# Kernel tuning notes

Measured on AMD Instinct MI355X. Metric: run time of the kernel, lower is better.

The kernel has to match this reference:

```python
import jax, jax.numpy as jnp
import numpy as np

NUM_HEADS = 32
NUM_KV_HEADS = 8
HEAD_DIM = 128
WINDOW = 512
NUM_META = 4


def _swa_sink_mask(S):
    # allowed = causal & (within sliding window OR sink/meta token)
    i = jnp.arange(S)[:, None]   # q_idx
    j = jnp.arange(S)[None, :]   # kv_idx
    return (i >= j) & (((i - j) <= WINDOW) | (j < NUM_META))


def setup_inputs() -> dict:
    key = jax.random.key(0)
    k1, k2, k3 = jax.random.split(key, 3)
    B, S = 1, 2048
    return {
        "query_states": jax.random.normal(k1, (B, S, NUM_HEADS * HEAD_DIM), dtype=jnp.float32),
        "key_states": jax.random.normal(k2, (B, S, NUM_KV_HEADS * HEAD_DIM), dtype=jnp.float32),
        "value_states": jax.random.normal(k3, (B, S, NUM_KV_HEADS * HEAD_DIM), dtype=jnp.float32),
    }


def reference(query_states, key_states, value_states):
    B, S, _ = query_states.shape
    n_rep = NUM_HEADS // NUM_KV_HEADS
    # [B, H, S, D]
    q = query_states.reshape(B, S, NUM_HEADS, HEAD_DIM).transpose(0, 2, 1, 3)
    k = key_states.reshape(B, S, NUM_KV_HEADS, HEAD_DIM).transpose(0, 2, 1, 3)
    v = value_states.reshape(B, S, NUM_KV_HEADS, HEAD_DIM).transpose(0, 2, 1, 3)
    # repeat_kv: interleaved repeat along head dim (GQA)
    k = jnp.repeat(k, n_rep, axis=1)
    v = jnp.repeat(v, n_rep, axis=1)

    scale = 1.0 / jnp.sqrt(jnp.float32(HEAD_DIM))  # flex_attention default scale
    scores = jnp.einsum("bhqd,bhkd->bhqk", q, k) * scale
    mask = _swa_sink_mask(S)  # [S, S], every row has q_idx==kv_idx allowed
    scores = jnp.where(mask[None, None], scores, -jnp.inf)
    attn = jax.nn.softmax(scores, axis=-1)
    out = jnp.einsum("bhqk,bhkd->bhqd", attn, v)
    return out.transpose(0, 2, 1, 3).reshape(B, S, NUM_HEADS * HEAD_DIM)
```

## Files before the change

kernel.cpp:

```cpp
#include <hip/hip_runtime.h>
#include <math.h>

typedef __attribute__((ext_vector_type(8))) short bf16x8;
typedef __attribute__((ext_vector_type(16))) float f32x16;

#define WIN 512
#define META 4
#define QSCALE (0.08838834764831845f * 1.4426950408889634f)
#define MFIX2 20.197730572445487f

union U8 { int4 i4; bf16x8 bf; };

static __device__ __forceinline__ unsigned bf16_rne(float x) {
  unsigned u = __float_as_uint(x);
  return (u + 0x7FFFu + ((u >> 16) & 1u)) >> 16;
}
static __device__ __forceinline__ unsigned pk2_rne(float a, float b) {
  return bf16_rne(a) | (bf16_rne(b) << 16);
}
static __device__ __forceinline__ unsigned pk2_tr(float a, float b) {
  return (__float_as_uint(a) >> 16) | (__float_as_uint(b) & 0xFFFF0000u);
}
static __device__ __forceinline__ void gload16(const void* g, void* l) {
  __builtin_amdgcn_global_load_lds(
      (const __attribute__((address_space(1))) unsigned int*)g,
      (__attribute__((address_space(3))) unsigned int*)l, 16, 0, 0);
}

__global__ __launch_bounds__(256) void swa_prep(
    const float* __restrict__ Kg, const float* __restrict__ Vg,
    unsigned short* __restrict__ Kw, unsigned short* __restrict__ Vw)
{
  __shared__ float Kf[64][132];
  __shared__ float Vf[64][132];
  const int tid = threadIdx.x;
  const int hk = blockIdx.x & 7, tj = blockIdx.x >> 3;
  const int j0 = tj * 64;
  const int krow = tid >> 5;
  const int f4c = tid & 31;
  #pragma unroll
  for (int r = 0; r < 8; ++r) {
    const int key = r * 8 + krow;
    *(float4*)&Kf[key][f4c * 4] =
        *(const float4*)(Kg + (size_t)(j0 + key) * 1024 + hk * 128 + f4c * 4);
    *(float4*)&Vf[key][f4c * 4] =
        *(const float4*)(Vg + (size_t)(j0 + key) * 1024 + hk * 128 + f4c * 4);
  }
  __syncthreads();
  unsigned short* kout = Kw + ((size_t)(hk * 32 + tj)) * 8192;
  #pragma unroll
  for (int p = 0; p < 4; ++p) {
    const int gid = p * 256 + tid;
    const int s = gid >> 6, key = gid & 63;
    const float* src = &Kf[key][s * 8];
    *(int4*)(kout + gid * 8) = make_int4(
        (int)pk2_tr(src[0], src[1]), (int)pk2_tr(src[2], src[3]),
        (int)pk2_tr(src[4], src[5]), (int)pk2_tr(src[6], src[7]));
  }
  unsigned short* vout = Vw + ((size_t)(hk * 32 + tj)) * 8192;
  #pragma unroll
  for (int p = 0; p < 4; ++p) {
    const int fid = p * 256 + tid;
    const int c = fid >> 7, dim = fid & 127;
    const int kb = 16 * (c >> 1) + 4 * (c & 1);
    *(int4*)(vout + fid * 8) = make_int4(
        (int)pk2_tr(Vf[kb + 0][dim], Vf[kb + 1][dim]),
        (int)pk2_tr(Vf[kb + 2][dim], Vf[kb + 3][dim]),
        (int)pk2_tr(Vf[kb + 8][dim], Vf[kb + 9][dim]),
        (int)pk2_tr(Vf[kb + 10][dim], Vf[kb + 11][dim]));
  }
}

__global__ __launch_bounds__(512, 2) void swa_fused(
    const float* __restrict__ Qg, const unsigned short* __restrict__ Kw,
    const unsigned short* __restrict__ Vw, float* __restrict__ Og)
{
  __shared__ __align__(16) unsigned short KsB[2][8192];
  __shared__ __align__(16) unsigned short VtB[3][8192];

  const int tid = threadIdx.x;
  const int lane = tid & 63, wid = tid >> 6;
  const int cl = lane & 31, hl = lane >> 5;
  const int bid = blockIdx.x;
  const int hk = bid & 7;
  const int bq = bid >> 3;
  const int q0 = bq << 6;
  const int h = hk * 4 + (wid & 3);
  const int qw0 = q0 + ((wid >> 2) << 5);

  int4 qf[8];
  {
    const float* qrow = Qg + (size_t)(qw0 + cl) * 4096 + h * 128 + hl * 8;
    #pragma unroll
    for (int kc = 0; kc < 8; ++kc) {
      float4 x = *(const float4*)(qrow + kc * 16);
      float4 y = *(const float4*)(qrow + kc * 16 + 4);
      qf[kc] = make_int4(pk2_rne(x.x*QSCALE, x.y*QSCALE), pk2_rne(x.z*QSCALE, x.w*QSCALE),
                         pk2_rne(y.x*QSCALE, y.y*QSCALE), pk2_rne(y.z*QSCALE, y.w*QSCALE));
    }
  }

  f32x16 acc[4];
  #pragma unroll
  for (int nt = 0; nt < 4; ++nt)
    #pragma unroll
    for (int i = 0; i < 16; ++i) acc[nt][i] = 0.f;
  float lpA = 0.f, lpB = 0.f;

  const int jstart = (q0 > WIN) ? ((q0 - WIN) & ~63) : 0;
  const int sink = (jstart > 0) ? 1 : 0;
  const int niter = ((q0 + 63 - jstart) >> 6) + 1 + sink;
  const int tj0 = jstart >> 6;

  auto stage = [&](const int tj, unsigned short* kd, unsigned short* vd) {
    const size_t base = ((size_t)(hk * 32 + tj)) << 14;
    const char* ks = (const char*)Kw + base + tid * 16;
    gload16(ks, (char*)kd + tid * 16);
    gload16(ks + 8192, (char*)kd + tid * 16 + 8192);
    const char* vs = (const char*)Vw + base + tid * 16;
    gload16(vs, (char*)vd + tid * 16);
    gload16(vs + 8192, (char*)vd + tid * 16 + 8192);
  };

  #define MKA(P, o) make_int4( \
      (int)__builtin_amdgcn_perm(P[(o)+1], P[(o)+0], 0x07060302u), \
      (int)__builtin_amdgcn_perm(P[(o)+3], P[(o)+2], 0x07060302u), \
      (int)__builtin_amdgcn_perm(P[(o)+5], P[(o)+4], 0x07060302u), \
      (int)__builtin_amdgcn_perm(P[(o)+7], P[(o)+6], 0x07060302u))

  auto pv4 = [&](const unsigned short* Vb, const int kc, const int4 aw) {
    U8 a; a.i4 = aw;
    #pragma unroll
    for (int nt = 0; nt < 4; ++nt) {
      U8 b; b.i4 = *(const int4*)(Vb + kc * 2048 + hl * 1024 + nt * 256 + cl * 8);
      acc[nt] = __builtin_amdgcn_mfma_f32_32x32x16_bf16(a.bf, b.bf, acc[nt], 0, 0, 0);
    }
  };

  unsigned pu1[16];
  #pragma unroll
  for (int i = 0; i < 16; ++i) pu1[i] = 0u;

  stage(sink ? 0 : tj0, KsB[0], VtB[0]);
  __syncthreads();

  const unsigned short *kCur = KsB[0], *kNxt = KsB[1];
  const unsigned short *vPrv = VtB[2], *vCur = VtB[0], *vNxt = VtB[1];

  for (int t = 0; t < niter; ++t) {
    const bool isSink = (sink != 0) && (t == 0);
    const int jt = isSink ? 0 : jstart + ((t - sink) << 6);
    const bool needMask = (jt + 63 > qw0) || (qw0 + 31 - jt > WIN);

    if (t + 1 < niter)
      stage(tj0 + (t + 1 - sink), (unsigned short*)kNxt, (unsigned short*)vNxt);

    if (t > sink) {
      __builtin_amdgcn_s_setprio(1);
      pv4(vPrv, 2, MKA(pu1, 0));
      pv4(vPrv, 3, MKA(pu1, 8));
      __builtin_amdgcn_s_setprio(0);
    }

    f32x16 s0v, s1v;
    #pragma unroll
    for (int i = 0; i < 16; ++i) { s0v[i] = 0.f; s1v[i] = 0.f; }
    __builtin_amdgcn_s_setprio(1);
    if (isSink) {
      #pragma unroll
      for (int kc = 0; kc < 8; ++kc) {
        U8 b; b.i4 = qf[kc];
        U8 a0; a0.i4 = *(const int4*)(kCur + kc * 1024 + hl * 512 + cl * 8);
        s0v = __builtin_amdgcn_mfma_f32_32x32x16_bf16(a0.bf, b.bf, s0v, 0, 0, 0);
      }
    } else {
      #pragma unroll
      for (int kc = 0; kc < 8; ++kc) {
        U8 b; b.i4 = qf[kc];
        U8 a0; a0.i4 = *(const int4*)(kCur + kc * 1024 + hl * 512 + cl * 8);
        s0v = __builtin_amdgcn_mfma_f32_32x32x16_bf16(a0.bf, b.bf, s0v, 0, 0, 0);
        U8 a1; a1.i4 = *(const int4*)(kCur + kc * 1024 + hl * 512 + 256 + cl * 8);
        s1v = __builtin_amdgcn_mfma_f32_32x32x16_bf16(a1.bf, b.bf, s1v, 0, 0, 0);
      }
    }
    __builtin_amdgcn_s_setprio(0);

    unsigned pu0[16];
    const int q = qw0 + cl;
    #pragma unroll
    for (int ri = 0; ri < 16; ++ri) {
      const int koff = (ri & 3) + 8 * (ri >> 2) + 4 * hl;
      bool ok0 = true, ok1 = true;
      if (needMask) {
        const int k0v = jt + koff, k1v = jt + 32 + koff;
        ok0 = (q >= k0v) && (((q - k0v) <= WIN) || (k0v < META));
        ok1 = (q >= k1v) && (((q - k1v) <= WIN) || (k1v < META));
      }
      unsigned u0 = ok0 ? (__float_as_uint(__builtin_amdgcn_exp2f(s0v[ri] - MFIX2)) & 0xFFFF0000u) : 0u;
      pu0[ri] = u0;
      lpA += __uint_as_float(u0);
      if (!isSink) {
        unsigned u1 = ok1 ? (__float_as_uint(__builtin_amdgcn_exp2f(s1v[ri] - MFIX2)) & 0xFFFF0000u) : 0u;
        pu1[ri] = u1;
        lpB += __uint_as_float(u1);
      }
    }

    __builtin_amdgcn_s_setprio(1);
    pv4(vCur, 0, MKA(pu0, 0));
    if (!isSink) pv4(vCur, 1, MKA(pu0, 8));
    __builtin_amdgcn_s_setprio(0);

    __syncthreads();

    { const unsigned short* tk = kCur; kCur = kNxt; kNxt = tk; }
    { const unsigned short* tv = vPrv; vPrv = vCur; vCur = vNxt; vNxt = tv; }
  }

  pv4(vPrv, 2, MKA(pu1, 0));
  pv4(vPrv, 3, MKA(pu1, 8));
  #undef MKA

  const float lp = lpA + lpB;
  const float ltot = lp + __shfl_xor(lp, 32);
  const float inv = __fdividef(1.0f, ltot);
  #pragma unroll
  for (int ri = 0; ri < 16; ++ri) {
    const int rl = (ri & 3) + 8 * (ri >> 2) + 4 * hl;
    const float invq = __shfl(inv, rl, 64);
    #pragma unroll
    for (int nt = 0; nt < 4; ++nt) {
      Og[(size_t)(qw0 + rl) * 4096 + h * 128 + nt * 32 + cl] = acc[nt][ri] * invq;
    }
  }
}

extern "C" void kernel_launch(void* const* d_in, const int* in_sizes, int n_in,
                              void* d_out, int out_size, void* d_ws, size_t ws_size,
                              hipStream_t stream) {
  const float* Q = (const float*)d_in[0];
  const float* K = (const float*)d_in[1];
  const float* V = (const float*)d_in[2];
  float* O = (float*)d_out;
  unsigned short* Kw = (unsigned short*)d_ws;
  unsigned short* Vw = Kw + (size_t)8 * 32 * 8192;
  hipLaunchKernelGGL(swa_prep, dim3(256), dim3(256), 0, stream, K, V, Kw, Vw);
  hipLaunchKernelGGL(swa_fused, dim3(256), dim3(512), 0, stream, Q, Kw, Vw, O);
}
```

Baseline: 123.4 us.

## Split head dimension across two wave groups with 1024-thread blocks

```diff
diff --git a/kernel.cpp b/kernel.cpp
--- a/kernel.cpp
+++ b/kernel.cpp
@@ -71,12 +71,12 @@
   }
 }
 
-__global__ __launch_bounds__(512, 2) void swa_fused(
+__global__ __launch_bounds__(1024, 4) void swa_fused(
     const float* __restrict__ Qg, const unsigned short* __restrict__ Kw,
     const unsigned short* __restrict__ Vw, float* __restrict__ Og)
 {
   __shared__ __align__(16) unsigned short KsB[2][8192];
-  __shared__ __align__(16) unsigned short VtB[3][8192];
+  __shared__ __align__(16) unsigned short VtB[2][8192];
 
   const int tid = threadIdx.x;
   const int lane = tid & 63, wid = tid >> 6;
@@ -86,7 +86,8 @@
   const int bq = bid >> 3;
   const int q0 = bq << 6;
   const int h = hk * 4 + (wid & 3);
-  const int qw0 = q0 + ((wid >> 2) << 5);
+  const int qw0 = q0 + (((wid >> 2) & 1) << 5);
+  const int dh = wid >> 3;
 
   int4 qf[8];
   {
@@ -100,9 +101,9 @@
     }
   }
 
-  f32x16 acc[4];
-  #pragma unroll
-  for (int nt = 0; nt < 4; ++nt)
+  f32x16 acc[2];
+  #pragma unroll
+  for (int nt = 0; nt < 2; ++nt)
     #pragma unroll
     for (int i = 0; i < 16; ++i) acc[nt][i] = 0.f;
   float lpA = 0.f, lpB = 0.f;
@@ -114,12 +115,8 @@
 
   auto stage = [&](const int tj, unsigned short* kd, unsigned short* vd) {
     const size_t base = ((size_t)(hk * 32 + tj)) << 14;
-    const char* ks = (const char*)Kw + base + tid * 16;
-    gload16(ks, (char*)kd + tid * 16);
-    gload16(ks + 8192, (char*)kd + tid * 16 + 8192);
-    const char* vs = (const char*)Vw + base + tid * 16;
-    gload16(vs, (char*)vd + tid * 16);
-    gload16(vs + 8192, (char*)vd + tid * 16 + 8192);
+    gload16((const char*)Kw + base + tid * 16, (char*)kd + tid * 16);
+    gload16((const char*)Vw + base + tid * 16, (char*)vd + tid * 16);
   };
 
   #define MKA(P, o) make_int4( \
@@ -128,97 +125,75 @@
       (int)__builtin_amdgcn_perm(P[(o)+5], P[(o)+4], 0x07060302u), \
       (int)__builtin_amdgcn_perm(P[(o)+7], P[(o)+6], 0x07060302u))
 
-  auto pv4 = [&](const unsigned short* Vb, const int kc, const int4 aw) {
-    U8 a; a.i4 = aw;
-    #pragma unroll
-    for (int nt = 0; nt < 4; ++nt) {
-      U8 b; b.i4 = *(const int4*)(Vb + kc * 2048 + hl * 1024 + nt * 256 + cl * 8);
-      acc[nt] = __builtin_amdgcn_mfma_f32_32x32x16_bf16(a.bf, b.bf, acc[nt], 0, 0, 0);
-    }
-  };
-
-  unsigned pu1[16];
-  #pragma unroll
-  for (int i = 0; i < 16; ++i) pu1[i] = 0u;
-
   stage(sink ? 0 : tj0, KsB[0], VtB[0]);
   __syncthreads();
-
-  const unsigned short *kCur = KsB[0], *kNxt = KsB[1];
-  const unsigned short *vPrv = VtB[2], *vCur = VtB[0], *vNxt = VtB[1];
 
   for (int t = 0; t < niter; ++t) {
     const bool isSink = (sink != 0) && (t == 0);
     const int jt = isSink ? 0 : jstart + ((t - sink) << 6);
-    const bool needMask = (jt + 63 > qw0) || (qw0 + 31 - jt > WIN);
+    const int cb = t & 1;
+    const unsigned short* kCur = KsB[cb];
+    const unsigned short* vCur = VtB[cb];
 
     if (t + 1 < niter)
-      stage(tj0 + (t + 1 - sink), (unsigned short*)kNxt, (unsigned short*)vNxt);
-
-    if (t > sink) {
+      stage(tj0 + (t + 1 - sink), KsB[cb ^ 1], VtB[cb ^ 1]);
+
+    const int nhb = isSink ? 1 : 2;
+    for (int hb = 0; hb < nhb; ++hb) {
+      const int jts = jt + (hb << 5);
+
+      f32x16 sv;
+      #pragma unroll
+      for (int i = 0; i < 16; ++i) sv[i] = 0.f;
       __builtin_amdgcn_s_setprio(1);
-      pv4(vPrv, 2, MKA(pu1, 0));
-      pv4(vPrv, 3, MKA(pu1, 8));
-      __builtin_amdgcn_s_setprio(0);
-    }
-
-    f32x16 s0v, s1v;
-    #pragma unroll
-    for (int i = 0; i < 16; ++i) { s0v[i] = 0.f; s1v[i] = 0.f; }
-    __builtin_amdgcn_s_setprio(1);
-    if (isSink) {
       #pragma unroll
       for (int kc = 0; kc < 8; ++kc) {
         U8 b; b.i4 = qf[kc];
-        U8 a0; a0.i4 = *(const int4*)(kCur + kc * 1024 + hl * 512 + cl * 8);
-        s0v = __builtin_amdgcn_mfma_f32_32x32x16_bf16(a0.bf, b.bf, s0v, 0, 0, 0);
+        U8 a; a.i4 = *(const int4*)(kCur + kc * 1024 + hl * 512 + (hb << 8) + cl * 8);
+        sv = __builtin_amdgcn_mfma_f32_32x32x16_bf16(a.bf, b.bf, sv, 0, 0, 0);
       }
-    } else {
+      __builtin_amdgcn_s_setprio(0);
+
+      const bool needMask = (jts + 31 > qw0) || (qw0 + 31 - jts > WIN);
+      unsigned pu[16];
+      float lpH = 0.f;
+      const int q = qw0 + cl;
       #pragma unroll
-      for (int kc = 0; kc < 8; ++kc) {
-        U8 b; b.i4 = qf[kc];
-        U8 a0; a0.i4 = *(const int4*)(kCur + kc * 1024 + hl * 512 + cl * 8);
-        s0v = __builtin_amdgcn_mfma_f32_32x32x16_bf16(a0.bf, b.bf, s0v, 0, 0, 0);
-        U8 a1; a1.i4 = *(const int4*)(kCur + kc * 1024 + hl * 512 + 256 + cl * 8);
-        s1v = __builtin_amdgcn_mfma_f32_32x32x16_bf16(a1.bf, b.bf, s1v, 0, 0, 0);
+      for (int ri = 0; ri < 16; ++ri) {
+        const int koff = (ri & 3) + 8 * (ri >> 2) + 4 * hl;
+        bool ok = true;
+        if (needMask) {
+          const int kv = jts + koff;
+          ok = (q >= kv) && (((q - kv) <= WIN) || (kv < META));
+        }
+        unsigned u = ok ? (__float_as_uint(__builtin_amdgcn_exp2f(sv[ri] - MFIX2)) & 0xFFFF0000u) : 0u;
+        pu[ri] = u;
+        lpH += __uint_as_float(u);
       }
+      (hb ? lpB : lpA) += lpH;
+
+      __builtin_amdgcn_s_setprio(1);
+      {
+        U8 a0; a0.i4 = MKA(pu, 0);
+        #pragma unroll
+        for (int nt2 = 0; nt2 < 2; ++nt2) {
+          U8 b; b.i4 = *(const int4*)(vCur + (2 * hb) * 2048 + hl * 1024 +
+                                      (2 * dh + nt2) * 256 + cl * 8);
+          acc[nt2] = __builtin_amdgcn_mfma_f32_32x32x16_bf16(a0.bf, b.bf, acc[nt2], 0, 0, 0);
+        }
+        U8 a1; a1.i4 = MKA(pu, 8);
+        #pragma unroll
+        for (int nt2 = 0; nt2 < 2; ++nt2) {
+          U8 b; b.i4 = *(const int4*)(vCur + (2 * hb + 1) * 2048 + hl * 1024 +
+                                      (2 * dh + nt2) * 256 + cl * 8);
+          acc[nt2] = __builtin_amdgcn_mfma_f32_32x32x16_bf16(a1.bf, b.bf, acc[nt2], 0, 0, 0);
+        }
+      }
+      __builtin_amdgcn_s_setprio(0);
     }
-    __builtin_amdgcn_s_setprio(0);
-
-    unsigned pu0[16];
-    const int q = qw0 + cl;
-    #pragma unroll
-    for (int ri = 0; ri < 16; ++ri) {
-      const int koff = (ri & 3) + 8 * (ri >> 2) + 4 * hl;
-      bool ok0 = true, ok1 = true;
-      if (needMask) {
-        const int k0v = jt + koff, k1v = jt + 32 + koff;
-        ok0 = (q >= k0v) && (((q - k0v) <= WIN) || (k0v < META));
-        ok1 = (q >= k1v) && (((q - k1v) <= WIN) || (k1v < META));
-      }
-      unsigned u0 = ok0 ? (__float_as_uint(__builtin_amdgcn_exp2f(s0v[ri] - MFIX2)) & 0xFFFF0000u) : 0u;
-      pu0[ri] = u0;
-      lpA += __uint_as_float(u0);
-      if (!isSink) {
-        unsigned u1 = ok1 ? (__float_as_uint(__builtin_amdgcn_exp2f(s1v[ri] - MFIX2)) & 0xFFFF0000u) : 0u;
-        pu1[ri] = u1;
-        lpB += __uint_as_float(u1);
-      }
-    }
-
-    __builtin_amdgcn_s_setprio(1);
-    pv4(vCur, 0, MKA(pu0, 0));
-    if (!isSink) pv4(vCur, 1, MKA(pu0, 8));
-    __builtin_amdgcn_s_setprio(0);
 
     __syncthreads();
-
-    { const unsigned short* tk = kCur; kCur = kNxt; kNxt = tk; }
-    { const unsigned short* tv = vPrv; vPrv = vCur; vCur = vNxt; vNxt = tv; }
-  }
-
-  pv4(vPrv, 2, MKA(pu1, 0));
-  pv4(vPrv, 3, MKA(pu1, 8));
+  }
   #undef MKA
 
   const float lp = lpA + lpB;
@@ -229,8 +204,9 @@
     const int rl = (ri & 3) + 8 * (ri >> 2) + 4 * hl;
     const float invq = __shfl(inv, rl, 64);
     #pragma unroll
-    for (int nt = 0; nt < 4; ++nt) {
-      Og[(size_t)(qw0 + rl) * 4096 + h * 128 + nt * 32 + cl] = acc[nt][ri] * invq;
+    for (int nt2 = 0; nt2 < 2; ++nt2) {
+      Og[(size_t)(qw0 + rl) * 4096 + h * 128 + dh * 64 + nt2 * 32 + cl] =
+          acc[nt2][ri] * invq;
     }
   }
 }
@@ -245,5 +221,5 @@
   unsigned short* Kw = (unsigned short*)d_ws;
   unsigned short* Vw = Kw + (size_t)8 * 32 * 8192;
   hipLaunchKernelGGL(swa_prep, dim3(256), dim3(256), 0, stream, K, V, Kw, Vw);
-  hipLaunchKernelGGL(swa_fused, dim3(256), dim3(512), 0, stream, Q, Kw, Vw, O);
-}
+  hipLaunchKernelGGL(swa_fused, dim3(256), dim3(1024), 0, stream, Q, Kw, Vw, O);
+}
```

Result: slower. 190.8 us (+54.6%).

## Deepen K/V LDS pipeline to prefetch two tiles ahead with vmcnt waits

Applied to the files above, without the earlier changes.

```diff
diff --git a/kernel.cpp b/kernel.cpp
--- a/kernel.cpp
+++ b/kernel.cpp
@@ -75,8 +75,8 @@
     const float* __restrict__ Qg, const unsigned short* __restrict__ Kw,
     const unsigned short* __restrict__ Vw, float* __restrict__ Og)
 {
-  __shared__ __align__(16) unsigned short KsB[2][8192];
-  __shared__ __align__(16) unsigned short VtB[3][8192];
+  __shared__ __align__(16) unsigned short KsB[3][8192];
+  __shared__ __align__(16) unsigned short VtB[4][8192];
 
   const int tid = threadIdx.x;
   const int lane = tid & 63, wid = tid >> 6;
@@ -112,8 +112,11 @@
   const int niter = ((q0 + 63 - jstart) >> 6) + 1 + sink;
   const int tj0 = jstart >> 6;
 
-  auto stage = [&](const int tj, unsigned short* kd, unsigned short* vd) {
+  auto stageT = [&](const int t) {
+    const int tj = (sink && t == 0) ? 0 : tj0 + t - sink;
     const size_t base = ((size_t)(hk * 32 + tj)) << 14;
+    unsigned short* kd = KsB[t % 3];
+    unsigned short* vd = VtB[t % 4];
     const char* ks = (const char*)Kw + base + tid * 16;
     gload16(ks, (char*)kd + tid * 16);
     gload16(ks + 8192, (char*)kd + tid * 16 + 8192);
@@ -141,21 +144,28 @@
   #pragma unroll
   for (int i = 0; i < 16; ++i) pu1[i] = 0u;
 
-  stage(sink ? 0 : tj0, KsB[0], VtB[0]);
-  __syncthreads();
-
-  const unsigned short *kCur = KsB[0], *kNxt = KsB[1];
-  const unsigned short *vPrv = VtB[2], *vCur = VtB[0], *vNxt = VtB[1];
+  stageT(0);
+  if (niter > 1) stageT(1);
 
   for (int t = 0; t < niter; ++t) {
     const bool isSink = (sink != 0) && (t == 0);
     const int jt = isSink ? 0 : jstart + ((t - sink) << 6);
     const bool needMask = (jt + 63 > qw0) || (qw0 + 31 - jt > WIN);
-
-    if (t + 1 < niter)
-      stage(tj0 + (t + 1 - sink), (unsigned short*)kNxt, (unsigned short*)vNxt);
+    const unsigned short* kCur = KsB[t % 3];
+    const unsigned short* vCur = VtB[t % 4];
+
+    if (t < niter - 1) {
+      asm volatile("s_waitcnt vmcnt(4)" ::: "memory");
+    } else {
+      asm volatile("s_waitcnt vmcnt(0)" ::: "memory");
+    }
+    __builtin_amdgcn_s_barrier();
+    __builtin_amdgcn_sched_barrier(0);
+
+    if (t + 2 < niter) stageT(t + 2);
 
     if (t > sink) {
+      const unsigned short* vPrv = VtB[(t - 1) % 4];
       __builtin_amdgcn_s_setprio(1);
       pv4(vPrv, 2, MKA(pu1, 0));
       pv4(vPrv, 3, MKA(pu1, 8));
@@ -210,15 +220,13 @@
     pv4(vCur, 0, MKA(pu0, 0));
     if (!isSink) pv4(vCur, 1, MKA(pu0, 8));
     __builtin_amdgcn_s_setprio(0);
-
-    __syncthreads();
-
-    { const unsigned short* tk = kCur; kCur = kNxt; kNxt = tk; }
-    { const unsigned short* tv = vPrv; vPrv = vCur; vCur = vNxt; vNxt = tv; }
-  }
-
-  pv4(vPrv, 2, MKA(pu1, 0));
-  pv4(vPrv, 3, MKA(pu1, 8));
+  }
+
+  {
+    const unsigned short* vPrv = VtB[(niter - 1) % 4];
+    pv4(vPrv, 2, MKA(pu1, 0));
+    pv4(vPrv, 3, MKA(pu1, 8));
+  }
   #undef MKA
 
   const float lp = lpA + lpB;
```

Result: no change. 121.4 us (-1.7%).
